# Optimization experiments

Hardware: AMD Instinct MI355X
Metric: run time of the kernel (lower is better)

## Reference

```python
import jax, jax.numpy as jnp
import numpy as np

B, SIDES, L = 8192, 2, 64   # batch, (left,right) trees, leaves per tree (complete binary tree)
V, D, C, R = 10000, 128, 128, 7  # vocab, word_dim, cpr_dim, num_rels


def setup_inputs() -> dict:
    key = jax.random.key(0)
    ks = jax.random.split(key, 9)
    s = 0.05
    return {
        "tokens": jax.random.randint(ks[0], (B, SIDES, L), 0, V, dtype=jnp.int32),
        "voc_w": jax.random.normal(ks[1], (V, D), dtype=jnp.float32) * s,
        "voc_b": jax.random.normal(ks[2], (D,), dtype=jnp.float32) * s,
        "cps_w": jax.random.normal(ks[3], (D, 2 * D), dtype=jnp.float32) * s,
        "cps_b": jax.random.normal(ks[4], (D,), dtype=jnp.float32) * s,
        "cpr_w": jax.random.normal(ks[5], (C, 2 * D), dtype=jnp.float32) * s,
        "cpr_b": jax.random.normal(ks[6], (C,), dtype=jnp.float32) * s,
        "sm_w": jax.random.normal(ks[7], (R, C), dtype=jnp.float32) * s,
        "sm_b": jax.random.normal(ks[8], (R,), dtype=jnp.float32) * s,
    }


def reference(tokens, voc_w, voc_b, cps_w, cps_b, cpr_w, cpr_b, sm_w, sm_b):
    # Leaf composition: one-hot @ Linear(voc_size, word_dim) == embedding gather + bias
    h = voc_w[tokens] + voc_b  # [B, 2, L, D]
    # Level-by-level composition of complete binary trees: cat(left,right) -> cps -> tanh
    n = h.shape[2]
    while n > 1:
        h = h.reshape(h.shape[0], SIDES, n // 2, 2 * h.shape[-1])  # adjacent pairs -> concat
        h = jnp.tanh(jnp.einsum('bsnk,dk->bsnd', h, cps_w) + cps_b)
        n //= 2
    root = h.reshape(h.shape[0], -1)  # [B, 2*D]: cat(left_cps, right_cps)
    z = jax.nn.leaky_relu(root @ cpr_w.T + cpr_b)  # LeakyReLU default slope 0.01
    return jax.nn.softmax(z @ sm_w.T + sm_b, axis=-1)  # [B, R]
```

## Files before the change

kernel.cpp:

```cpp
#include <hip/hip_runtime.h>
#include <hip/hip_bf16.h>


typedef __attribute__((ext_vector_type(8))) short bf16x8;
typedef __attribute__((ext_vector_type(4))) float f32x4;

#define VOCN (10000 * 128)
#define CPSN (128 * 256)
#define CPRN (128 * 256)

__device__ __forceinline__ uint pk2(float a, float b) {
  union { __hip_bfloat162 h2; uint u; } cv;
  cv.h2 = __float22bfloat162_rn(make_float2(a, b));
  return cv.u;
}
__device__ __forceinline__ float2 up2(uint u) {
  union { uint u; __hip_bfloat162 h2; } cv; cv.u = u;
  return __bfloat1622float2(cv.h2);
}
__device__ __forceinline__ float fast_tanh(float x) {
  float e = __builtin_amdgcn_exp2f(x * 2.88539008f);
  return 1.0f - 2.0f * __builtin_amdgcn_rcpf(e + 1.0f);
}
__device__ __forceinline__ int sf(int r) { return r ^ ((r >> 3) & 7); }

__global__ void prep_kernel(const float* __restrict__ voc_w, const float* __restrict__ voc_b,
                            const float* __restrict__ cps_w, const float* __restrict__ cpr_w,
                            ushort* __restrict__ ws) {
  const int i4 = (blockIdx.x * 256 + threadIdx.x) * 4;
  if (i4 >= VOCN + CPSN + CPRN) return;
  float4 v;
  if (i4 < VOCN) {
    v = *(const float4*)(voc_w + i4);
    const float4 bb = *(const float4*)(voc_b + (i4 & 127));
    v.x += bb.x; v.y += bb.y; v.z += bb.z; v.w += bb.w;
  } else if (i4 < VOCN + CPSN) {
    v = *(const float4*)(cps_w + (i4 - VOCN));
  } else {
    v = *(const float4*)(cpr_w + (i4 - VOCN - CPSN));
  }
  uint2 w; w.x = pk2(v.x, v.y); w.y = pk2(v.z, v.w);
  *(uint2*)(ws + i4) = w;
}

#define MFMA16(Ax, Bx, Cx) __builtin_amdgcn_mfma_f32_16x16x32_bf16(Ax, Bx, Cx, 0, 0, 0)

template<int TOFF>
__device__ __forceinline__ void tile16(const char* hb, const bf16x8 (&A)[2][8],
                                       int RL, int RR, f32x4& aA, f32x4& aB) {
  bf16x8 bl[4], br[4];
#pragma unroll
  for (int q = 0; q < 4; ++q) {
    bl[q] = *(const bf16x8*)(hb + RL + TOFF + q * 4096);
    br[q] = *(const bf16x8*)(hb + RR + TOFF + q * 4096);
  }
#pragma unroll
  for (int q = 0; q < 4; ++q) {
    aA = MFMA16(A[0][q], bl[q], aA);
    aB = MFMA16(A[1][q], bl[q], aB);
  }
#pragma unroll
  for (int q = 0; q < 4; ++q) {
    aA = MFMA16(A[0][4 + q], br[q], aA);
    aB = MFMA16(A[1][4 + q], br[q], aB);
  }
}

template<int TOFF>
__device__ __forceinline__ void wtile(char* hb, int W, const f32x4& aA, const f32x4& aB) {
  uint2 w0, w1;
  w0.x = pk2(fast_tanh(aA[0]), fast_tanh(aA[1]));
  w0.y = pk2(fast_tanh(aA[2]), fast_tanh(aA[3]));
  w1.x = pk2(fast_tanh(aB[0]), fast_tanh(aB[1]));
  w1.y = pk2(fast_tanh(aB[2]), fast_tanh(aB[3]));
  *(uint2*)(hb + W + TOFF) = w0;
  *(uint2*)(hb + W + TOFF + 2048) = w1;
}

template<int PRE>
__global__ __launch_bounds__(256, 4)
void trnn_kernel(const int* __restrict__ tokens,
                 const float* __restrict__ voc_w, const float* __restrict__ voc_b,
                 const float* __restrict__ cps_w, const float* __restrict__ cps_b,
                 const float* __restrict__ cpr_w, const float* __restrict__ cpr_b,
                 const float* __restrict__ sm_w, const float* __restrict__ sm_b,
                 const ushort* __restrict__ wsb, float* __restrict__ out) {
  __shared__ ushort h[16384];
  const int tid = threadIdx.x;
  const int lane = tid & 63, wv = tid >> 6;
  const int l15 = lane & 15, lh = lane >> 4;
  const int b = blockIdx.x;
  char* hb = (char*)h;

  const ushort* voc_bf = wsb;
  const ushort* cps_bf = wsb + VOCN;
  const ushort* cpr_bf = wsb + VOCN + CPSN;

  const int lhb = lh * 1024;
  const int RLa = lhb + sf(2 * l15) * 16;
  const int RRa = lhb + sf(2 * l15 + 1) * 16;
  const int RLb = lhb + sf(2 * l15 + 32) * 16;
  const int RRb = lhb + sf(2 * l15 + 33) * 16;
  const int RL3 = (((l15 >> 3) & 1) << 14) + lhb + sf((l15 & 7) * 2) * 16;
  const int RR3 = (((l15 >> 3) & 1) << 14) + lhb + sf((l15 & 7) * 2 + 1) * 16;
  const int RL4 = (((l15 >> 2) & 1) << 14) + lhb + sf((l15 & 3) * 2) * 16;
  const int RR4 = (((l15 >> 2) & 1) << 14) + lhb + sf((l15 & 3) * 2 + 1) * 16;
  const int RL5 = (((l15 >> 1) & 1) << 14) + lhb + sf((l15 & 1) * 2) * 16;
  const int RR5 = (((l15 >> 1) & 1) << 14) + lhb + sf((l15 & 1) * 2 + 1) * 16;
  const int RL6 = ((l15 & 1) << 14) + lhb;
  const int RR6 = ((l15 & 1) << 14) + lhb + 16;
  const int dpart = (((wv * 32 + lh * 4) >> 3) << 10) + ((lh & 1) << 3);
  const int Wa = sf(l15) * 16 + dpart;
  const int Wb = sf(l15 + 16) * 16 + dpart;
  const int W3 = (((l15 >> 3) & 1) << 14) + sf(l15 & 7) * 16 + dpart;
  const int W4 = (((l15 >> 2) & 1) << 14) + sf(l15 & 3) * 16 + dpart;
  const int W5 = (((l15 >> 1) & 1) << 14) + sf(l15 & 1) * 16 + dpart;
  const int W6 = ((l15 & 1) << 14) + dpart;

  bf16x8 A[2][8];
  f32x4 bias[2];
#pragma unroll
  for (int mt = 0; mt < 2; ++mt) {
    const int d = wv * 32 + mt * 16 + l15;
#pragma unroll
    for (int kt = 0; kt < 8; ++kt) {
      const int k = kt * 32 + lh * 8;
      if constexpr (PRE) {
        A[mt][kt] = *(const bf16x8*)(cps_bf + d * 256 + k);
      } else {
        const float* p = cps_w + d * 256 + k;
        float4 lo = *(const float4*)p, hi = *(const float4*)(p + 4);
        union { bf16x8 v; uint4 u; } f;
        f.u.x = pk2(lo.x, lo.y); f.u.y = pk2(lo.z, lo.w);
        f.u.z = pk2(hi.x, hi.y); f.u.w = pk2(hi.z, hi.w);
        A[mt][kt] = f.v;
      }
    }
    const float4 bb = *(const float4*)(cps_b + wv * 32 + mt * 16 + lh * 4);
    bias[mt][0] = bb.x; bias[mt][1] = bb.y; bias[mt][2] = bb.z; bias[mt][3] = bb.w;
  }

  {
    const int tree = tid >> 7, lf = (tid >> 1) & 63, half = tid & 1;
    const int tok = tokens[b * 128 + tree * 64 + lf];
    char* tp = hb + tree * 16384 + half * 8192 + sf(lf) * 16;
    if constexpr (PRE) {
      const ushort* vr = voc_bf + tok * 128 + half * 64;
#pragma unroll
      for (int j = 0; j < 8; ++j)
        *(uint4*)(tp + j * 1024) = *(const uint4*)(vr + j * 8);
    } else {
      const float* vw = voc_w + tok * 128 + half * 64;
      const float* vb = voc_b + half * 64;
#pragma unroll
      for (int j = 0; j < 8; ++j) {
        float4 v0 = *(const float4*)(vw + j * 8);
        float4 v1 = *(const float4*)(vw + j * 8 + 4);
        float4 q0 = *(const float4*)(vb + j * 8);
        float4 q1 = *(const float4*)(vb + j * 8 + 4);
        uint4 w;
        w.x = pk2(v0.x + q0.x, v0.y + q0.y);
        w.y = pk2(v0.z + q0.z, v0.w + q0.w);
        w.z = pk2(v1.x + q1.x, v1.y + q1.y);
        w.w = pk2(v1.z + q1.z, v1.w + q1.w);
        *(uint4*)(tp + j * 1024) = w;
      }
    }
  }
  __syncthreads();

  {
    f32x4 a0 = bias[0], b0 = bias[1], a1 = bias[0], b1 = bias[1];
    f32x4 a2 = bias[0], b2 = bias[1], a3 = bias[0], b3 = bias[1];
    tile16<0>(hb, A, RLa, RRa, a0, b0);
    tile16<0>(hb, A, RLb, RRb, a1, b1);
    tile16<16384>(hb, A, RLa, RRa, a2, b2);
    tile16<16384>(hb, A, RLb, RRb, a3, b3);
    __syncthreads();
    wtile<0>(hb, Wa, a0, b0);
    wtile<0>(hb, Wb, a1, b1);
    wtile<16384>(hb, Wa, a2, b2);
    wtile<16384>(hb, Wb, a3, b3);
    __syncthreads();
  }
  {
    f32x4 a0 = bias[0], b0 = bias[1], a1 = bias[0], b1 = bias[1];
    tile16<0>(hb, A, RLa, RRa, a0, b0);
    tile16<16384>(hb, A, RLa, RRa, a1, b1);
    __syncthreads();
    wtile<0>(hb, Wa, a0, b0);
    wtile<16384>(hb, Wa, a1, b1);
    __syncthreads();
  }
  {
    f32x4 a0 = bias[0], b0 = bias[1];
    tile16<0>(hb, A, RL3, RR3, a0, b0);
    __syncthreads();
    wtile<0>(hb, W3, a0, b0);
    __syncthreads();
  }
  {
    f32x4 a0 = bias[0], b0 = bias[1];
    tile16<0>(hb, A, RL4, RR4, a0, b0);
    __syncthreads();
    if (l15 < 8) wtile<0>(hb, W4, a0, b0);
    __syncthreads();
  }
  {
    f32x4 a0 = bias[0], b0 = bias[1];
    tile16<0>(hb, A, RL5, RR5, a0, b0);
    __syncthreads();
    if (l15 < 4) wtile<0>(hb, W5, a0, b0);
    __syncthreads();
  }
  {
    f32x4 a0 = bias[0], b0 = bias[1];
    tile16<0>(hb, A, RL6, RR6, a0, b0);
    __syncthreads();
    if (l15 < 2) wtile<0>(hb, W6, a0, b0);
    __syncthreads();
  }


  {
    const int half = tid >> 7, c = tid & 127;
    const char* rp = hb + half * 16384;
    float acc = 0.f;
#pragma unroll 4
    for (int ch = 0; ch < 16; ++ch) {
      uint4 u = *(const uint4*)(rp + ch * 1024);
      float2 e0 = up2(u.x), e1 = up2(u.y), e2 = up2(u.z), e3 = up2(u.w);
      if constexpr (PRE) {
        uint4 wq = *(const uint4*)(cpr_bf + c * 256 + half * 128 + ch * 8);
        float2 w0 = up2(wq.x), w1 = up2(wq.y), w2 = up2(wq.z), w3 = up2(wq.w);
        acc += e0.x * w0.x + e0.y * w0.y + e1.x * w1.x + e1.y * w1.y
             + e2.x * w2.x + e2.y * w2.y + e3.x * w3.x + e3.y * w3.y;
      } else {
        const float* wr = cpr_w + c * 256 + half * 128 + ch * 8;
        float4 w0 = *(const float4*)wr, w1 = *(const float4*)(wr + 4);
        acc += e0.x * w0.x + e0.y * w0.y + e1.x * w0.z + e1.y * w0.w
             + e2.x * w1.x + e2.y * w1.y + e3.x * w1.z + e3.y * w1.w;
      }
    }
    *(float*)(hb + ((tid >> 4) << 10) + 512 + ((tid & 15) << 2)) = acc;
  }
  __syncthreads();
  if (tid < 128) {
    const float p0 = *(const float*)(hb + ((tid >> 4) << 10) + 512 + ((tid & 15) << 2));
    const int j1 = tid + 128;
    const float p1 = *(const float*)(hb + ((j1 >> 4) << 10) + 512 + ((j1 & 15) << 2));
    float z = p0 + p1 + cpr_b[tid];
    z = z > 0.f ? z : 0.01f * z;
    *(float*)(hb + 16384 + ((tid >> 3) << 10) + 768 + ((tid & 7) << 2)) = z;
  }
  __syncthreads();

  if (wv == 0) {
    const int i0 = lane, i1 = 64 + lane;
    const float za = *(const float*)(hb + 16384 + ((i0 >> 3) << 10) + 768 + ((i0 & 7) << 2));
    const float zc = *(const float*)(hb + 16384 + ((i1 >> 3) << 10) + 768 + ((i1 & 7) << 2));
    float p[7];
#pragma unroll
    for (int j = 0; j < 7; ++j)
      p[j] = za * sm_w[j * 128 + lane] + zc * sm_w[j * 128 + 64 + lane];
#pragma unroll
    for (int j = 0; j < 7; ++j) {
      float v = p[j];
#pragma unroll
      for (int off = 32; off >= 1; off >>= 1) v += __shfl_xor(v, off, 64);
      p[j] = v + sm_b[j];
    }
    float mx = p[0];
#pragma unroll
    for (int j = 1; j < 7; ++j) mx = fmaxf(mx, p[j]);
    float e[7], s = 0.f;
#pragma unroll
    for (int j = 0; j < 7; ++j) { e[j] = __expf(p[j] - mx); s += e[j]; }
    const float inv = 1.f / s;
    if (lane == 0) {
#pragma unroll
      for (int j = 0; j < 7; ++j) out[b * 7 + j] = e[j] * inv;
    }
  }
}

extern "C" void kernel_launch(void* const* d_in, const int* in_sizes, int n_in,
                              void* d_out, int out_size, void* d_ws, size_t ws_size,
                              hipStream_t stream) {
  const int*   tokens = (const int*)  d_in[0];
  const float* voc_w  = (const float*)d_in[1];
  const float* voc_b  = (const float*)d_in[2];
  const float* cps_w  = (const float*)d_in[3];
  const float* cps_b  = (const float*)d_in[4];
  const float* cpr_w  = (const float*)d_in[5];
  const float* cpr_b  = (const float*)d_in[6];
  const float* sm_w   = (const float*)d_in[7];
  const float* sm_b   = (const float*)d_in[8];
  float* out = (float*)d_out;

  const int B = in_sizes[0] / 128;
  const size_t need = (size_t)(VOCN + CPSN + CPRN) * sizeof(ushort);

  if (ws_size >= need) {
    ushort* ws = (ushort*)d_ws;
    const int tot4 = (VOCN + CPSN + CPRN) / 4;
    prep_kernel<<<(tot4 + 255) / 256, 256, 0, stream>>>(voc_w, voc_b, cps_w, cpr_w, ws);
    trnn_kernel<1><<<B, 256, 0, stream>>>(tokens, voc_w, voc_b, cps_w, cps_b,
                                          cpr_w, cpr_b, sm_w, sm_b, ws, out);
  } else {
    trnn_kernel<0><<<B, 256, 0, stream>>>(tokens, voc_w, voc_b, cps_w, cps_b,
                                          cpr_w, cpr_b, sm_w, sm_b,
                                          (const ushort*)d_ws, out);
  }
}
```

Before: 161.5 us.

## Process two batch rows per block with prefetched second-row embeddings

Each block now handles two batch elements in sequence, so the per-block loading and bf16 packing of the cps weight fragments into registers is amortized over two trees. The embedding rows for the second element are loaded into registers before the first element's tree reduction and written to shared memory afterwards, hiding gather latency. The first root is stashed and restored so the cpr projection and softmax run once for both rows, with one thread per output feature and no cross-half reduction. The grid is halved, which lowers available parallelism and adds register pressure from the prefetch buffer.

```diff
diff --git a/kernel.cpp b/kernel.cpp
--- a/kernel.cpp
+++ b/kernel.cpp
@@ -45,6 +45,11 @@
 
 #define MFMA16(Ax, Bx, Cx) __builtin_amdgcn_mfma_f32_16x16x32_bf16(Ax, Bx, Cx, 0, 0, 0)
 
+struct Bases {
+  int RLa, RRa, RLb, RRb, RL3, RR3, RL4, RR4, RL5, RR5, RL6, RR6;
+  int Wa, Wb, W3, W4, W5, W6;
+};
+
 template<int TOFF>
 __device__ __forceinline__ void tile16(const char* hb, const bf16x8 (&A)[2][8],
                                        int RL, int RR, f32x4& aA, f32x4& aB) {
@@ -75,6 +80,62 @@
   w1.y = pk2(fast_tanh(aB[2]), fast_tanh(aB[3]));
   *(uint2*)(hb + W + TOFF) = w0;
   *(uint2*)(hb + W + TOFF + 2048) = w1;
+}
+
+__device__ __forceinline__ void run_levels(char* hb, const bf16x8 (&A)[2][8],
+                                           const f32x4 (&bias)[2], const Bases& B,
+                                           int l15) {
+  {
+    f32x4 a0 = bias[0], b0 = bias[1], a1 = bias[0], b1 = bias[1];
+    f32x4 a2 = bias[0], b2 = bias[1], a3 = bias[0], b3 = bias[1];
+    tile16<0>(hb, A, B.RLa, B.RRa, a0, b0);
+    tile16<0>(hb, A, B.RLb, B.RRb, a1, b1);
+    tile16<16384>(hb, A, B.RLa, B.RRa, a2, b2);
+    tile16<16384>(hb, A, B.RLb, B.RRb, a3, b3);
+    __syncthreads();
+    wtile<0>(hb, B.Wa, a0, b0);
+    wtile<0>(hb, B.Wb, a1, b1);
+    wtile<16384>(hb, B.Wa, a2, b2);
+    wtile<16384>(hb, B.Wb, a3, b3);
+    __syncthreads();
+  }
+  {
+    f32x4 a0 = bias[0], b0 = bias[1], a1 = bias[0], b1 = bias[1];
+    tile16<0>(hb, A, B.RLa, B.RRa, a0, b0);
+    tile16<16384>(hb, A, B.RLa, B.RRa, a1, b1);
+    __syncthreads();
+    wtile<0>(hb, B.Wa, a0, b0);
+    wtile<16384>(hb, B.Wa, a1, b1);
+    __syncthreads();
+  }
+  {
+    f32x4 a0 = bias[0], b0 = bias[1];
+    tile16<0>(hb, A, B.RL3, B.RR3, a0, b0);
+    __syncthreads();
+    wtile<0>(hb, B.W3, a0, b0);
+    __syncthreads();
+  }
+  {
+    f32x4 a0 = bias[0], b0 = bias[1];
+    tile16<0>(hb, A, B.RL4, B.RR4, a0, b0);
+    __syncthreads();
+    if (l15 < 8) wtile<0>(hb, B.W4, a0, b0);
+    __syncthreads();
+  }
+  {
+    f32x4 a0 = bias[0], b0 = bias[1];
+    tile16<0>(hb, A, B.RL5, B.RR5, a0, b0);
+    __syncthreads();
+    if (l15 < 4) wtile<0>(hb, B.W5, a0, b0);
+    __syncthreads();
+  }
+  {
+    f32x4 a0 = bias[0], b0 = bias[1];
+    tile16<0>(hb, A, B.RL6, B.RR6, a0, b0);
+    __syncthreads();
+    if (l15 < 2) wtile<0>(hb, B.W6, a0, b0);
+    __syncthreads();
+  }
 }
 
 template<int PRE>
@@ -89,33 +150,36 @@
   const int tid = threadIdx.x;
   const int lane = tid & 63, wv = tid >> 6;
   const int l15 = lane & 15, lh = lane >> 4;
-  const int b = blockIdx.x;
+  const int b0 = blockIdx.x * 2;
   char* hb = (char*)h;
 
   const ushort* voc_bf = wsb;
   const ushort* cps_bf = wsb + VOCN;
   const ushort* cpr_bf = wsb + VOCN + CPSN;
 
-  const int lhb = lh * 1024;
-  const int RLa = lhb + sf(2 * l15) * 16;
-  const int RRa = lhb + sf(2 * l15 + 1) * 16;
-  const int RLb = lhb + sf(2 * l15 + 32) * 16;
-  const int RRb = lhb + sf(2 * l15 + 33) * 16;
-  const int RL3 = (((l15 >> 3) & 1) << 14) + lhb + sf((l15 & 7) * 2) * 16;
-  const int RR3 = (((l15 >> 3) & 1) << 14) + lhb + sf((l15 & 7) * 2 + 1) * 16;
-  const int RL4 = (((l15 >> 2) & 1) << 14) + lhb + sf((l15 & 3) * 2) * 16;
-  const int RR4 = (((l15 >> 2) & 1) << 14) + lhb + sf((l15 & 3) * 2 + 1) * 16;
-  const int RL5 = (((l15 >> 1) & 1) << 14) + lhb + sf((l15 & 1) * 2) * 16;
-  const int RR5 = (((l15 >> 1) & 1) << 14) + lhb + sf((l15 & 1) * 2 + 1) * 16;
-  const int RL6 = ((l15 & 1) << 14) + lhb;
-  const int RR6 = ((l15 & 1) << 14) + lhb + 16;
-  const int dpart = (((wv * 32 + lh * 4) >> 3) << 10) + ((lh & 1) << 3);
-  const int Wa = sf(l15) * 16 + dpart;
-  const int Wb = sf(l15 + 16) * 16 + dpart;
-  const int W3 = (((l15 >> 3) & 1) << 14) + sf(l15 & 7) * 16 + dpart;
-  const int W4 = (((l15 >> 2) & 1) << 14) + sf(l15 & 3) * 16 + dpart;
-  const int W5 = (((l15 >> 1) & 1) << 14) + sf(l15 & 1) * 16 + dpart;
-  const int W6 = ((l15 & 1) << 14) + dpart;
+  Bases Bs;
+  {
+    const int lhb = lh * 1024;
+    Bs.RLa = lhb + sf(2 * l15) * 16;
+    Bs.RRa = lhb + sf(2 * l15 + 1) * 16;
+    Bs.RLb = lhb + sf(2 * l15 + 32) * 16;
+    Bs.RRb = lhb + sf(2 * l15 + 33) * 16;
+    Bs.RL3 = (((l15 >> 3) & 1) << 14) + lhb + sf((l15 & 7) * 2) * 16;
+    Bs.RR3 = (((l15 >> 3) & 1) << 14) + lhb + sf((l15 & 7) * 2 + 1) * 16;
+    Bs.RL4 = (((l15 >> 2) & 1) << 14) + lhb + sf((l15 & 3) * 2) * 16;
+    Bs.RR4 = (((l15 >> 2) & 1) << 14) + lhb + sf((l15 & 3) * 2 + 1) * 16;
+    Bs.RL5 = (((l15 >> 1) & 1) << 14) + lhb + sf((l15 & 1) * 2) * 16;
+    Bs.RR5 = (((l15 >> 1) & 1) << 14) + lhb + sf((l15 & 1) * 2 + 1) * 16;
+    Bs.RL6 = ((l15 & 1) << 14) + lhb;
+    Bs.RR6 = ((l15 & 1) << 14) + lhb + 16;
+    const int dpart = (((wv * 32 + lh * 4) >> 3) << 10) + ((lh & 1) << 3);
+    Bs.Wa = sf(l15) * 16 + dpart;
+    Bs.Wb = sf(l15 + 16) * 16 + dpart;
+    Bs.W3 = (((l15 >> 3) & 1) << 14) + sf(l15 & 7) * 16 + dpart;
+    Bs.W4 = (((l15 >> 2) & 1) << 14) + sf(l15 & 3) * 16 + dpart;
+    Bs.W5 = (((l15 >> 1) & 1) << 14) + sf(l15 & 1) * 16 + dpart;
+    Bs.W6 = ((l15 & 1) << 14) + dpart;
+  }
 
   bf16x8 A[2][8];
   f32x4 bias[2];
@@ -140,125 +204,113 @@
     bias[mt][0] = bb.x; bias[mt][1] = bb.y; bias[mt][2] = bb.z; bias[mt][3] = bb.w;
   }
 
-  {
-    const int tree = tid >> 7, lf = (tid >> 1) & 63, half = tid & 1;
-    const int tok = tokens[b * 128 + tree * 64 + lf];
-    char* tp = hb + tree * 16384 + half * 8192 + sf(lf) * 16;
-    if constexpr (PRE) {
-      const ushort* vr = voc_bf + tok * 128 + half * 64;
-#pragma unroll
-      for (int j = 0; j < 8; ++j)
-        *(uint4*)(tp + j * 1024) = *(const uint4*)(vr + j * 8);
-    } else {
-      const float* vw = voc_w + tok * 128 + half * 64;
-      const float* vb = voc_b + half * 64;
-#pragma unroll
-      for (int j = 0; j < 8; ++j) {
-        float4 v0 = *(const float4*)(vw + j * 8);
-        float4 v1 = *(const float4*)(vw + j * 8 + 4);
-        float4 q0 = *(const float4*)(vb + j * 8);
-        float4 q1 = *(const float4*)(vb + j * 8 + 4);
-        uint4 w;
-        w.x = pk2(v0.x + q0.x, v0.y + q0.y);
-        w.y = pk2(v0.z + q0.z, v0.w + q0.w);
-        w.z = pk2(v1.x + q1.x, v1.y + q1.y);
-        w.w = pk2(v1.z + q1.z, v1.w + q1.w);
-        *(uint4*)(tp + j * 1024) = w;
+  const int tree_e = tid >> 7, lf_e = (tid >> 1) & 63, half_e = tid & 1;
+  char* tp = hb + tree_e * 16384 + half_e * 8192 + sf(lf_e) * 16;
+  const int tok0 = tokens[b0 * 128 + tree_e * 64 + lf_e];
+  const int tok1 = tokens[(b0 + 1) * 128 + tree_e * 64 + lf_e];
+  uint4 pf[8];
+  if constexpr (PRE) {
+    const ushort* vr0 = voc_bf + tok0 * 128 + half_e * 64;
+#pragma unroll
+    for (int j = 0; j < 8; ++j)
+      *(uint4*)(tp + j * 1024) = *(const uint4*)(vr0 + j * 8);
+    const ushort* vr1 = voc_bf + tok1 * 128 + half_e * 64;
+#pragma unroll
+    for (int j = 0; j < 8; ++j)
+      pf[j] = *(const uint4*)(vr1 + j * 8);
+  } else {
+    const float* vw = voc_w + tok0 * 128 + half_e * 64;
+    const float* vb = voc_b + half_e * 64;
+#pragma unroll
+    for (int j = 0; j < 8; ++j) {
+      float4 v0 = *(const float4*)(vw + j * 8);
+      float4 v1 = *(const float4*)(vw + j * 8 + 4);
+      float4 q0 = *(const float4*)(vb + j * 8);
+      float4 q1 = *(const float4*)(vb + j * 8 + 4);
+      uint4 w;
+      w.x = pk2(v0.x + q0.x, v0.y + q0.y);
+      w.y = pk2(v0.z + q0.z, v0.w + q0.w);
+      w.z = pk2(v1.x + q1.x, v1.y + q1.y);
+      w.w = pk2(v1.z + q1.z, v1.w + q1.w);
+      *(uint4*)(tp + j * 1024) = w;
+    }
+  }
+  __syncthreads();
+
+  run_levels(hb, A, bias, Bs, l15);
+
+  uint stash = 0;
+  if (tid < 128) {
+    const int T = tid >> 6, d2 = tid & 63;
+    stash = *(const uint*)(hb + T * 16384 + ((2 * d2) >> 3) * 1024 + ((2 * d2) & 7) * 2);
+  }
+  __syncthreads();
+
+  if constexpr (PRE) {
+#pragma unroll
+    for (int j = 0; j < 8; ++j)
+      *(uint4*)(tp + j * 1024) = pf[j];
+  } else {
+    const float* vw = voc_w + tok1 * 128 + half_e * 64;
+    const float* vb = voc_b + half_e * 64;
+#pragma unroll
+    for (int j = 0; j < 8; ++j) {
+      float4 v0 = *(const float4*)(vw + j * 8);
+      float4 v1 = *(const float4*)(vw + j * 8 + 4);
+      float4 q0 = *(const float4*)(vb + j * 8);
+      float4 q1 = *(const float4*)(vb + j * 8 + 4);
+      uint4 w;
+      w.x = pk2(v0.x + q0.x, v0.y + q0.y);
+      w.y = pk2(v0.z + q0.z, v0.w + q0.w);
+      w.z = pk2(v1.x + q1.x, v1.y + q1.y);
+      w.w = pk2(v1.z + q1.z, v1.w + q1.w);
+      *(uint4*)(tp + j * 1024) = w;
+    }
+  }
+  __syncthreads();
+
+  run_levels(hb, A, bias, Bs, l15);
+
+  if (tid < 128) {
+    const int T = tid >> 6, d2 = tid & 63;
+    *(uint*)(hb + T * 16384 + ((2 * d2) >> 3) * 1024 + 32 + ((2 * d2) & 7) * 2) = stash;
+  }
+  __syncthreads();
+
+  {
+    const int r = tid >> 7, c = tid & 127;
+    const int rbase = r ? 0 : 32;
+    float acc = 0.f;
+#pragma unroll
+    for (int t = 0; t < 2; ++t) {
+#pragma unroll 4
+      for (int ch = 0; ch < 16; ++ch) {
+        uint4 u = *(const uint4*)(hb + t * 16384 + ch * 1024 + rbase);
+        float2 e0 = up2(u.x), e1 = up2(u.y), e2 = up2(u.z), e3 = up2(u.w);
+        if constexpr (PRE) {
+          uint4 wq = *(const uint4*)(cpr_bf + c * 256 + t * 128 + ch * 8);
+          float2 w0 = up2(wq.x), w1 = up2(wq.y), w2 = up2(wq.z), w3 = up2(wq.w);
+          acc += e0.x * w0.x + e0.y * w0.y + e1.x * w1.x + e1.y * w1.y
+               + e2.x * w2.x + e2.y * w2.y + e3.x * w3.x + e3.y * w3.y;
+        } else {
+          const float* wr = cpr_w + c * 256 + t * 128 + ch * 8;
+          float4 w0 = *(const float4*)wr, w1 = *(const float4*)(wr + 4);
+          acc += e0.x * w0.x + e0.y * w0.y + e1.x * w0.z + e1.y * w0.w
+               + e2.x * w1.x + e2.y * w1.y + e3.x * w1.z + e3.y * w1.w;
+        }
       }
     }
-  }
-  __syncthreads();
-
-  {
-    f32x4 a0 = bias[0], b0 = bias[1], a1 = bias[0], b1 = bias[1];
-    f32x4 a2 = bias[0], b2 = bias[1], a3 = bias[0], b3 = bias[1];
-    tile16<0>(hb, A, RLa, RRa, a0, b0);
-    tile16<0>(hb, A, RLb, RRb, a1, b1);
-    tile16<16384>(hb, A, RLa, RRa, a2, b2);
-    tile16<16384>(hb, A, RLb, RRb, a3, b3);
-    __syncthreads();
-    wtile<0>(hb, Wa, a0, b0);
-    wtile<0>(hb, Wb, a1, b1);
-    wtile<16384>(hb, Wa, a2, b2);
-    wtile<16384>(hb, Wb, a3, b3);
-    __syncthreads();
-  }
-  {
-    f32x4 a0 = bias[0], b0 = bias[1], a1 = bias[0], b1 = bias[1];
-    tile16<0>(hb, A, RLa, RRa, a0, b0);
-    tile16<16384>(hb, A, RLa, RRa, a1, b1);
-    __syncthreads();
-    wtile<0>(hb, Wa, a0, b0);
-    wtile<16384>(hb, Wa, a1, b1);
-    __syncthreads();
-  }
-  {
-    f32x4 a0 = bias[0], b0 = bias[1];
-    tile16<0>(hb, A, RL3, RR3, a0, b0);
-    __syncthreads();
-    wtile<0>(hb, W3, a0, b0);
-    __syncthreads();
-  }
-  {
-    f32x4 a0 = bias[0], b0 = bias[1];
-    tile16<0>(hb, A, RL4, RR4, a0, b0);
-    __syncthreads();
-    if (l15 < 8) wtile<0>(hb, W4, a0, b0);
-    __syncthreads();
-  }
-  {
-    f32x4 a0 = bias[0], b0 = bias[1];
-    tile16<0>(hb, A, RL5, RR5, a0, b0);
-    __syncthreads();
-    if (l15 < 4) wtile<0>(hb, W5, a0, b0);
-    __syncthreads();
-  }
-  {
-    f32x4 a0 = bias[0], b0 = bias[1];
-    tile16<0>(hb, A, RL6, RR6, a0, b0);
-    __syncthreads();
-    if (l15 < 2) wtile<0>(hb, W6, a0, b0);
-    __syncthreads();
-  }
-
-
-  {
-    const int half = tid >> 7, c = tid & 127;
-    const char* rp = hb + half * 16384;
-    float acc = 0.f;
-#pragma unroll 4
-    for (int ch = 0; ch < 16; ++ch) {
-      uint4 u = *(const uint4*)(rp + ch * 1024);
-      float2 e0 = up2(u.x), e1 = up2(u.y), e2 = up2(u.z), e3 = up2(u.w);
-      if constexpr (PRE) {
-        uint4 wq = *(const uint4*)(cpr_bf + c * 256 + half * 128 + ch * 8);
-        float2 w0 = up2(wq.x), w1 = up2(wq.y), w2 = up2(wq.z), w3 = up2(wq.w);
-        acc += e0.x * w0.x + e0.y * w0.y + e1.x * w1.x + e1.y * w1.y
-             + e2.x * w2.x + e2.y * w2.y + e3.x * w3.x + e3.y * w3.y;
-      } else {
-        const float* wr = cpr_w + c * 256 + half * 128 + ch * 8;
-        float4 w0 = *(const float4*)wr, w1 = *(const float4*)(wr + 4);
-        acc += e0.x * w0.x + e0.y * w0.y + e1.x * w0.z + e1.y * w0.w
-             + e2.x * w1.x + e2.y * w1.y + e3.x * w1.z + e3.y * w1.w;
-      }
-    }
-    *(float*)(hb + ((tid >> 4) << 10) + 512 + ((tid & 15) << 2)) = acc;
-  }
-  __syncthreads();
-  if (tid < 128) {
-    const float p0 = *(const float*)(hb + ((tid >> 4) << 10) + 512 + ((tid & 15) << 2));
-    const int j1 = tid + 128;
-    const float p1 = *(const float*)(hb + ((j1 >> 4) << 10) + 512 + ((j1 & 15) << 2));
-    float z = p0 + p1 + cpr_b[tid];
+    float z = acc + cpr_b[c];
     z = z > 0.f ? z : 0.01f * z;
-    *(float*)(hb + 16384 + ((tid >> 3) << 10) + 768 + ((tid & 7) << 2)) = z;
-  }
-  __syncthreads();
-
-  if (wv == 0) {
-    const int i0 = lane, i1 = 64 + lane;
-    const float za = *(const float*)(hb + 16384 + ((i0 >> 3) << 10) + 768 + ((i0 & 7) << 2));
-    const float zc = *(const float*)(hb + 16384 + ((i1 >> 3) << 10) + 768 + ((i1 & 7) << 2));
+    *(float*)(hb + r * 16384 + ((c >> 3) << 10) + 768 + ((c & 7) << 2)) = z;
+  }
+  __syncthreads();
+
+  if (wv < 2) {
+    const char* zb = hb + wv * 16384;
+    const int i1 = 64 + lane;
+    const float za = *(const float*)(zb + ((lane >> 3) << 10) + 768 + ((lane & 7) << 2));
+    const float zc = *(const float*)(zb + ((i1 >> 3) << 10) + 768 + ((i1 & 7) << 2));
     float p[7];
 #pragma unroll
     for (int j = 0; j < 7; ++j)
@@ -279,7 +331,7 @@
     const float inv = 1.f / s;
     if (lane == 0) {
 #pragma unroll
-      for (int j = 0; j < 7; ++j) out[b * 7 + j] = e[j] * inv;
+      for (int j = 0; j < 7; ++j) out[(b0 + wv) * 7 + j] = e[j] * inv;
     }
   }
 }
@@ -305,11 +357,11 @@
     ushort* ws = (ushort*)d_ws;
     const int tot4 = (VOCN + CPSN + CPRN) / 4;
     prep_kernel<<<(tot4 + 255) / 256, 256, 0, stream>>>(voc_w, voc_b, cps_w, cpr_w, ws);
-    trnn_kernel<1><<<B, 256, 0, stream>>>(tokens, voc_w, voc_b, cps_w, cps_b,
-                                          cpr_w, cpr_b, sm_w, sm_b, ws, out);
+    trnn_kernel<1><<<B / 2, 256, 0, stream>>>(tokens, voc_w, voc_b, cps_w, cps_b,
+                                              cpr_w, cpr_b, sm_w, sm_b, ws, out);
   } else {
-    trnn_kernel<0><<<B, 256, 0, stream>>>(tokens, voc_w, voc_b, cps_w, cps_b,
-                                          cpr_w, cpr_b, sm_w, sm_b,
-                                          (const ushort*)d_ws, out);
-  }
-}
+    trnn_kernel<0><<<B / 2, 256, 0, stream>>>(tokens, voc_w, voc_b, cps_w, cps_b,
+                                              cpr_w, cpr_b, sm_w, sm_b,
+                                              (const ushort*)d_ws, out);
+  }
+}
```

Result: slower. 196.8 us (+21.8%).
